# Performance work log

Hardware: AMD Instinct MI355X
Metric: run time of the kernel (lower is better)

Reference implementation:

```python
import jax, jax.numpy as jnp
import numpy as np

DIM = 1024
NUM_HEADS = 16
REL_DIM = 32
B, N = 8, 512


def setup_inputs() -> dict:
    key = jax.random.key(0)
    ks = jax.random.split(key, 8)
    s = 0.02
    return {
        "x": jax.random.normal(ks[0], (B, N, DIM), dtype=jnp.float32),
        "rel_bias": jax.random.normal(ks[1], (B, N, N, REL_DIM), dtype=jnp.float32),
        # torch nn.Linear convention: weight (out_features, in_features)
        "W_qkv": jax.random.normal(ks[2], (3 * DIM, DIM), dtype=jnp.float32) * s,
        "b_qkv": jax.random.normal(ks[3], (3 * DIM,), dtype=jnp.float32) * s,
        "W_rel": jax.random.normal(ks[4], (NUM_HEADS, REL_DIM), dtype=jnp.float32) * s,
        "b_rel": jax.random.normal(ks[5], (NUM_HEADS,), dtype=jnp.float32) * s,
        "W_out": jax.random.normal(ks[6], (DIM, DIM), dtype=jnp.float32) * s,
        "b_out": jax.random.normal(ks[7], (DIM,), dtype=jnp.float32) * s,
    }


def reference(x, rel_bias, W_qkv, b_qkv, W_rel, b_rel, W_out, b_out):
    Bx, Nx, D = x.shape
    H = NUM_HEADS
    hd = D // H
    # QKV projection: (B,N,3D) -> (B,N,3,H,hd)
    qkv = (x @ W_qkv.T + b_qkv).reshape(Bx, Nx, 3, H, hd)
    q, k, v = qkv[:, :, 0], qkv[:, :, 1], qkv[:, :, 2]
    scale = hd ** -0.5
    attn = jnp.einsum('bnhd,bmhd->bhnm', q, k) * scale
    # per-pair relative bias projected to heads: (B,N,N,H) -> (B,H,N,N)
    rel = (rel_bias @ W_rel.T + b_rel).transpose(0, 3, 1, 2)
    attn = jax.nn.softmax(attn + rel, axis=-1)
    out = jnp.einsum('bhnm,bmhd->bnhd', attn, v).reshape(Bx, Nx, D)
    return out @ W_out.T + b_out
```

## Files before the change

kernel.cpp:

```cpp
#include <hip/hip_runtime.h>

typedef unsigned short u16;
typedef unsigned int u32;
typedef __attribute__((ext_vector_type(8))) __bf16 bf16x8;
typedef __attribute__((ext_vector_type(4))) float f32x4;

union U8 {
  bf16x8 b;
  uint2 u2[2];
  uint4 u4;
  u16 us[8];
};

__device__ __forceinline__ u16 f2bf(float f) {
  u32 x = __float_as_uint(f);
  x += 0x7FFFu + ((x >> 16) & 1u);
  return (u16)(x >> 16);
}
__device__ __forceinline__ float bf2f(u16 u) {
  return __uint_as_float(((u32)u) << 16);
}

#define GLOAD16(gp, lp)                                                          \
  __builtin_amdgcn_global_load_lds(                                              \
      (const __attribute__((address_space(1))) unsigned int*)(const void*)(gp),  \
      (__attribute__((address_space(3))) unsigned int*)(void*)(lp), 16, 0, 0)

__global__ void k_convert_all(const float* __restrict__ x, const float* __restrict__ wq,
                              const float* __restrict__ wo, u16* __restrict__ xb,
                              u16* __restrict__ wqb, u16* __restrict__ wob) {
  const int NX = 1048576, NQ = 786432, NO = 262144;
  int idx = blockIdx.x * blockDim.x + threadIdx.x;
  int stride = gridDim.x * blockDim.x;
  for (int i = idx; i < NX + NQ + NO; i += stride) {
    const float4* s;
    ushort4* d;
    int k;
    if (i < NX) { s = (const float4*)x; d = (ushort4*)xb; k = i; }
    else if (i < NX + NQ) { s = (const float4*)wq; d = (ushort4*)wqb; k = i - NX; }
    else { s = (const float4*)wo; d = (ushort4*)wob; k = i - NX - NQ; }
    float4 v = s[k];
    ushort4 o;
    o.x = f2bf(v.x); o.y = f2bf(v.y); o.z = f2bf(v.z); o.w = f2bf(v.w);
    d[k] = o;
  }
}

__global__ __launch_bounds__(256) void k_rel(const float* __restrict__ rb,
                                             const float* __restrict__ Wr,
                                             const float* __restrict__ br,
                                             u16* __restrict__ out) {
  __shared__ float Wl[16][32];
  __shared__ float bl[16];
  int t = threadIdx.x;
  ((float*)Wl)[t] = Wr[t];
  ((float*)Wl)[t + 256] = Wr[t + 256];
  if (t < 16) bl[t] = br[t];
  __syncthreads();

  const int i16 = t & 15, j = (t >> 4) & 3, c = t >> 6;
  const int mt = blockIdx.x, ntg = blockIdx.y, b = blockIdx.z;
  const int nt = ntg >> 2, g = ntg & 3;
  const int n = nt * 16 + 4 * g + j;
  const int m = mt * 64 + c * 16 + i16;

  const float4* rp = (const float4*)(rb + ((size_t)(b * 512 + n) * 512 + m) * 32);
  float4 r4[8];
#pragma unroll
  for (int q = 0; q < 8; ++q) r4[q] = rp[q];

  const size_t obase =
      (((size_t)(b * 16) * 32 + nt) * 8 + mt) * 1024 + c * 256 + (g * 16 + i16) * 4 + j;
#pragma unroll
  for (int h = 0; h < 16; ++h) {
    float acc = bl[h];
    const float* w = Wl[h];
#pragma unroll
    for (int q = 0; q < 8; ++q) {
      acc += r4[q].x * w[4 * q + 0] + r4[q].y * w[4 * q + 1] +
             r4[q].z * w[4 * q + 2] + r4[q].w * w[4 * q + 3];
    }
    out[obase + (size_t)h * 262144] = f2bf(acc);
  }
}

template <int MODE>
__global__ __launch_bounds__(256) void k_gemm(const u16* __restrict__ A,
                                              const u16* __restrict__ Bm,
                                              const float* __restrict__ bias,
                                              u16* __restrict__ Qo, u16* __restrict__ Ko,
                                              u16* __restrict__ Vo, float* __restrict__ Co,
                                              int K) {
  __shared__ u16 Al[128 * 64];
  __shared__ u16 Bl[128 * 64];
  const int t = threadIdx.x;
  const int lane = t & 63, wid = t >> 6;
  const int g = lane >> 4, i16 = lane & 15;
  const int wm = wid >> 1, wn = wid & 1;
  const int bm = blockIdx.y, bn = blockIdx.x;

  f32x4 zero = {0.f, 0.f, 0.f, 0.f};
  f32x4 acc[4][4];
#pragma unroll
  for (int mi = 0; mi < 4; ++mi)
#pragma unroll
    for (int ni = 0; ni < 4; ++ni) acc[mi][ni] = zero;

  int srow[4], sgc[4];
#pragma unroll
  for (int i = 0; i < 4; ++i) {
    int ch = wid * 256 + i * 64 + lane;
    int r = ch >> 3, cs = ch & 7;
    srow[i] = r;
    sgc[i] = cs ^ (r & 7);
  }

  for (int k0 = 0; k0 < K; k0 += 64) {
    __syncthreads();
#pragma unroll
    for (int i = 0; i < 4; ++i) {
      const u16* ga = A + (size_t)(bm * 128 + srow[i]) * K + k0 + sgc[i] * 8;
      const u16* gb = Bm + (size_t)(bn * 128 + srow[i]) * K + k0 + sgc[i] * 8;
      GLOAD16(ga, Al + (size_t)(wid * 256 + i * 64) * 8);
      GLOAD16(gb, Bl + (size_t)(wid * 256 + i * 64) * 8);
    }
    __syncthreads();

#pragma unroll
    for (int kk = 0; kk < 2; ++kk) {
      U8 af[4], bfr[4];
#pragma unroll
      for (int mi = 0; mi < 4; ++mi) {
        int row = wm * 64 + mi * 16 + i16;
        int ch = (g + 4 * kk) ^ (row & 7);
        af[mi].u4 = *(const uint4*)(Al + row * 64 + ch * 8);
      }
#pragma unroll
      for (int ni = 0; ni < 4; ++ni) {
        int row = wn * 64 + ni * 16 + i16;
        int ch = (g + 4 * kk) ^ (row & 7);
        bfr[ni].u4 = *(const uint4*)(Bl + row * 64 + ch * 8);
      }
#pragma unroll
      for (int mi = 0; mi < 4; ++mi)
#pragma unroll
        for (int ni = 0; ni < 4; ++ni)
          acc[mi][ni] = __builtin_amdgcn_mfma_f32_16x16x32_bf16(af[mi].b, bfr[ni].b,
                                                                acc[mi][ni], 0, 0, 0);
    }
  }

#pragma unroll
  for (int mi = 0; mi < 4; ++mi) {
#pragma unroll
    for (int ni = 0; ni < 4; ++ni) {
      int colb = bn * 128 + wn * 64 + ni * 16;
      int col = colb + i16;
#pragma unroll
      for (int j = 0; j < 4; ++j) {
        int row = bm * 128 + wm * 64 + mi * 16 + 4 * g + j;
        float v = acc[mi][ni][j] + bias[col];
        if (MODE == 0) {
          int tt = col >> 10;
          int h = (col >> 6) & 15;
          int d = col & 63;
          int b = row >> 9;
          int n = row & 511;
          u16* dst = (tt == 0) ? Qo : ((tt == 1) ? Ko : Vo);
          dst[((size_t)(b * 16 + h) * 512 + n) * 64 + d] = f2bf(v);
        } else {
          Co[(size_t)row * 1024 + col] = v;
        }
      }
    }
  }
}

__global__ __launch_bounds__(256) void k_vt(const u16* __restrict__ V, u16* __restrict__ Vt) {
  __shared__ u16 Tl[64][72];
  const int t = threadIdx.x;
  const int n0 = blockIdx.x * 64;
  const size_t bh = blockIdx.y;
#pragma unroll
  for (int i = 0; i < 2; ++i) {
    int c = i * 256 + t;
    int r = c >> 3, c8 = (c & 7) * 8;
    U8 v;
    v.u4 = *(const uint4*)(V + (bh * 512 + n0 + r) * 64 + c8);
    *(uint2*)&Tl[r][c8] = v.u2[0];
    *(uint2*)&Tl[r][c8 + 4] = v.u2[1];
  }
  __syncthreads();
#pragma unroll
  for (int i = 0; i < 2; ++i) {
    int c = i * 256 + t;
    int d = c >> 3, n8 = (c & 7) * 8;
    U8 o;
#pragma unroll
    for (int j = 0; j < 8; ++j) o.us[j] = Tl[n8 + j][d];
    *(uint4*)(Vt + (bh * 64 + d) * 512 + n0 + n8) = o.u4;
  }
}

__global__ __launch_bounds__(256) void k_attn(const u16* __restrict__ Q,
                                              const u16* __restrict__ Kb,
                                              const u16* __restrict__ Vtb,
                                              const u16* __restrict__ Rel,
                                              u16* __restrict__ Out) {
  __shared__ u16 Kl[2][64 * 64];
  __shared__ u16 Vl[2][64 * 64];
  __shared__ u16 Pl[4][16 * 68];

  const int qt = blockIdx.x, h = blockIdx.y, b = blockIdx.z;
  const int t = threadIdx.x, lane = t & 63, wid = t >> 6;
  const int g = lane >> 4, i16 = lane & 15;
  const size_t bh = (size_t)(b * 16 + h);

  const u16* Qg = Q + (bh * 512 + qt * 64 + wid * 16 + i16) * 64;
  U8 qf[2];
  qf[0].u4 = *(const uint4*)(Qg + 8 * g);
  qf[1].u4 = *(const uint4*)(Qg + 8 * g + 32);

  float m_run[4], l_run[4];
  f32x4 zero = {0.f, 0.f, 0.f, 0.f};
  f32x4 acc[4];
#pragma unroll
  for (int c = 0; c < 4; ++c) acc[c] = zero;
#pragma unroll
  for (int j = 0; j < 4; ++j) { m_run[j] = -1e30f; l_run[j] = 0.f; }

  int srow[2], sgc[2];
#pragma unroll
  for (int i = 0; i < 2; ++i) {
    int ch = wid * 128 + i * 64 + lane;
    int r = ch >> 3, cs = ch & 7;
    srow[i] = r;
    sgc[i] = cs ^ (r & 7);
  }

  const u16* Kg0 = Kb + bh * 512 * 64;
  const u16* Vg0 = Vtb + bh * 64 * 512;
  const u16* Rg = Rel + ((bh * 32 + qt * 4 + wid) * 8) * 1024 + lane * 4;

#define STAGE(buf, m0)                                                                  \
  do {                                                                                  \
    _Pragma("unroll") for (int i = 0; i < 2; ++i) {                                     \
      GLOAD16(Kg0 + (size_t)((m0) + srow[i]) * 64 + sgc[i] * 8,                         \
              &Kl[buf][(size_t)(wid * 128 + i * 64) * 8]);                              \
      GLOAD16(Vg0 + (size_t)srow[i] * 512 + (m0) + sgc[i] * 8,                          \
              &Vl[buf][(size_t)(wid * 128 + i * 64) * 8]);                              \
    }                                                                                   \
  } while (0)

  STAGE(0, 0);
  __syncthreads();

  for (int it = 0; it < 8; ++it) {
    const int buf = it & 1;
    if (it < 7) STAGE(buf ^ 1, it * 64 + 64);

    uint2 rl[4];
#pragma unroll
    for (int c = 0; c < 4; ++c) rl[c] = *(const uint2*)(Rg + it * 1024 + c * 256);

    f32x4 s[4];
#pragma unroll
    for (int c = 0; c < 4; ++c) s[c] = zero;
    __builtin_amdgcn_s_setprio(1);
#pragma unroll
    for (int c = 0; c < 4; ++c) {
#pragma unroll
      for (int kk = 0; kk < 2; ++kk) {
        int row = c * 16 + i16;
        int ch = (g + 4 * kk) ^ (row & 7);
        U8 kf;
        kf.u4 = *(const uint4*)(&Kl[buf][row * 64 + ch * 8]);
        s[c] = __builtin_amdgcn_mfma_f32_16x16x32_bf16(qf[kk].b, kf.b, s[c], 0, 0, 0);
      }
    }
    __builtin_amdgcn_s_setprio(0);

#pragma unroll
    for (int c = 0; c < 4; ++c) {
      const u16* rc = (const u16*)&rl[c];
#pragma unroll
      for (int j = 0; j < 4; ++j) s[c][j] = s[c][j] * 0.125f + bf2f(rc[j]);
    }
    float fac[4];
#pragma unroll
    for (int j = 0; j < 4; ++j) {
      float pm = fmaxf(fmaxf(s[0][j], s[1][j]), fmaxf(s[2][j], s[3][j]));
      pm = fmaxf(pm, __shfl_xor(pm, 1));
      pm = fmaxf(pm, __shfl_xor(pm, 2));
      pm = fmaxf(pm, __shfl_xor(pm, 4));
      pm = fmaxf(pm, __shfl_xor(pm, 8));
      float mnew = fmaxf(m_run[j], pm);
      fac[j] = __expf(m_run[j] - mnew);
      m_run[j] = mnew;
    }
#pragma unroll
    for (int c = 0; c < 4; ++c)
#pragma unroll
      for (int j = 0; j < 4; ++j) s[c][j] = __expf(s[c][j] - m_run[j]);
#pragma unroll
    for (int j = 0; j < 4; ++j) {
      float rs = s[0][j] + s[1][j] + s[2][j] + s[3][j];
      rs += __shfl_xor(rs, 1);
      rs += __shfl_xor(rs, 2);
      rs += __shfl_xor(rs, 4);
      rs += __shfl_xor(rs, 8);
      l_run[j] = l_run[j] * fac[j] + rs;
    }
#pragma unroll
    for (int c = 0; c < 4; ++c)
#pragma unroll
      for (int j = 0; j < 4; ++j) acc[c][j] *= fac[j];

    u16* Pw = Pl[wid];
#pragma unroll
    for (int c = 0; c < 4; ++c)
#pragma unroll
      for (int j = 0; j < 4; ++j)
        Pw[(4 * g + j) * 68 + c * 16 + i16] = f2bf(s[c][j]);
    __syncthreads();

    U8 pf[2];
#pragma unroll
    for (int kk = 0; kk < 2; ++kk) {
      const u16* p = Pl[wid] + i16 * 68 + 8 * g + 32 * kk;
      pf[kk].u2[0] = *(const uint2*)p;
      pf[kk].u2[1] = *(const uint2*)(p + 4);
    }
    __builtin_amdgcn_s_setprio(1);
#pragma unroll
    for (int c = 0; c < 4; ++c) {
#pragma unroll
      for (int kk = 0; kk < 2; ++kk) {
        int row = c * 16 + i16;
        int ch = (g + 4 * kk) ^ (row & 7);
        U8 vf;
        vf.u4 = *(const uint4*)(&Vl[buf][row * 64 + ch * 8]);
        acc[c] = __builtin_amdgcn_mfma_f32_16x16x32_bf16(pf[kk].b, vf.b, acc[c], 0, 0, 0);
      }
    }
    __builtin_amdgcn_s_setprio(0);
    __syncthreads();
  }
#undef STAGE

#pragma unroll
  for (int c = 0; c < 4; ++c) {
#pragma unroll
    for (int j = 0; j < 4; ++j) {
      int n = qt * 64 + wid * 16 + 4 * g + j;
      float v = acc[c][j] / l_run[j];
      Out[((size_t)b * 512 + n) * 1024 + h * 64 + c * 16 + i16] = f2bf(v);
    }
  }
}

extern "C" void kernel_launch(void* const* d_in, const int* in_sizes, int n_in,
                              void* d_out, int out_size, void* d_ws, size_t ws_size,
                              hipStream_t stream) {
  const float* x = (const float*)d_in[0];
  const float* rel_bias = (const float*)d_in[1];
  const float* W_qkv = (const float*)d_in[2];
  const float* b_qkv = (const float*)d_in[3];
  const float* W_rel = (const float*)d_in[4];
  const float* b_rel = (const float*)d_in[5];
  const float* W_out = (const float*)d_in[6];
  const float* b_out = (const float*)d_in[7];
  float* out = (float*)d_out;

  char* ws = (char*)d_ws;
  u16* x_bf    = (u16*)(ws);
  u16* Vt      = (u16*)(ws);
  u16* wqkv_bf = (u16*)(ws + 8388608);
  u16* wout_bf = (u16*)(ws + 14680064);
  u16* Qw      = (u16*)(ws + 16777216);
  u16* Kw      = (u16*)(ws + 25165824);
  u16* Vw      = (u16*)(ws + 33554432);
  u16* relb    = (u16*)(ws + 41943040);
  u16* attno   = (u16*)(ws + 109051904);

  k_convert_all<<<2048, 256, 0, stream>>>(x, W_qkv, W_out, x_bf, wqkv_bf, wout_bf);

  k_rel<<<dim3(8, 128, 8), 256, 0, stream>>>(rel_bias, W_rel, b_rel, relb);

  k_gemm<0><<<dim3(24, 32), 256, 0, stream>>>(x_bf, wqkv_bf, b_qkv, Qw, Kw, Vw, nullptr, 1024);

  k_vt<<<dim3(8, 128), 256, 0, stream>>>(Vw, Vt);

  k_attn<<<dim3(8, 16, 8), 256, 0, stream>>>(Qw, Kw, Vt, relb, attno);

  k_gemm<1><<<dim3(8, 32), 256, 0, stream>>>(attno, wout_bf, b_out, nullptr, nullptr, nullptr,
                                             out, 1024);
}
```

Measured before the change: 202.4 us.

## Fuse V transpose into QKV GEMM epilogue and read rel weights directly

The QKV GEMM epilogue now writes V directly in transposed (d-major) layout, packing four consecutive rows into one 8-byte store, so the separate k_vt transpose kernel and its launch and round trip through memory are removed. k_rel drops its shared-memory staging of W_rel/b_rel and the block barrier, reading the weights directly from global memory, where they are expected to hit in cache. Writing V transposed gives strided, less coalesced stores in the GEMM epilogue, and the direct weight reads may add scalar or vector loads in place of LDS reads.

```diff
diff --git a/kernel.cpp b/kernel.cpp
--- a/kernel.cpp
+++ b/kernel.cpp
@@ -50,14 +50,7 @@
                                              const float* __restrict__ Wr,
                                              const float* __restrict__ br,
                                              u16* __restrict__ out) {
-  __shared__ float Wl[16][32];
-  __shared__ float bl[16];
-  int t = threadIdx.x;
-  ((float*)Wl)[t] = Wr[t];
-  ((float*)Wl)[t + 256] = Wr[t + 256];
-  if (t < 16) bl[t] = br[t];
-  __syncthreads();
-
+  const int t = threadIdx.x;
   const int i16 = t & 15, j = (t >> 4) & 3, c = t >> 6;
   const int mt = blockIdx.x, ntg = blockIdx.y, b = blockIdx.z;
   const int nt = ntg >> 2, g = ntg & 3;
@@ -73,8 +66,8 @@
       (((size_t)(b * 16) * 32 + nt) * 8 + mt) * 1024 + c * 256 + (g * 16 + i16) * 4 + j;
 #pragma unroll
   for (int h = 0; h < 16; ++h) {
-    float acc = bl[h];
-    const float* w = Wl[h];
+    float acc = br[h];
+    const float* w = Wr + h * 32;
 #pragma unroll
     for (int q = 0; q < 8; ++q) {
       acc += r4[q].x * w[4 * q + 0] + r4[q].y * w[4 * q + 1] +
@@ -154,51 +147,32 @@
   for (int mi = 0; mi < 4; ++mi) {
 #pragma unroll
     for (int ni = 0; ni < 4; ++ni) {
-      int colb = bn * 128 + wn * 64 + ni * 16;
-      int col = colb + i16;
-#pragma unroll
-      for (int j = 0; j < 4; ++j) {
-        int row = bm * 128 + wm * 64 + mi * 16 + 4 * g + j;
-        float v = acc[mi][ni][j] + bias[col];
-        if (MODE == 0) {
-          int tt = col >> 10;
-          int h = (col >> 6) & 15;
-          int d = col & 63;
-          int b = row >> 9;
-          int n = row & 511;
-          u16* dst = (tt == 0) ? Qo : ((tt == 1) ? Ko : Vo);
-          dst[((size_t)(b * 16 + h) * 512 + n) * 64 + d] = f2bf(v);
+      int col = bn * 128 + wn * 64 + ni * 16 + i16;
+      int row0 = bm * 128 + wm * 64 + mi * 16 + 4 * g;
+      float bia = bias[col];
+      if (MODE == 0) {
+        int tt = col >> 10;
+        int h = (col >> 6) & 15;
+        int d = col & 63;
+        int b = row0 >> 9;
+        int n0 = row0 & 511;
+        if (tt < 2) {
+          u16* dst = (tt == 0) ? Qo : Ko;
+#pragma unroll
+          for (int j = 0; j < 4; ++j)
+            dst[((size_t)(b * 16 + h) * 512 + n0 + j) * 64 + d] = f2bf(acc[mi][ni][j] + bia);
         } else {
-          Co[(size_t)row * 1024 + col] = v;
+          uint2 w;
+          w.x = (u32)f2bf(acc[mi][ni][0] + bia) | ((u32)f2bf(acc[mi][ni][1] + bia) << 16);
+          w.y = (u32)f2bf(acc[mi][ni][2] + bia) | ((u32)f2bf(acc[mi][ni][3] + bia) << 16);
+          *(uint2*)(Vo + ((size_t)(b * 16 + h) * 64 + d) * 512 + n0) = w;
         }
-      }
-    }
-  }
-}
-
-__global__ __launch_bounds__(256) void k_vt(const u16* __restrict__ V, u16* __restrict__ Vt) {
-  __shared__ u16 Tl[64][72];
-  const int t = threadIdx.x;
-  const int n0 = blockIdx.x * 64;
-  const size_t bh = blockIdx.y;
-#pragma unroll
-  for (int i = 0; i < 2; ++i) {
-    int c = i * 256 + t;
-    int r = c >> 3, c8 = (c & 7) * 8;
-    U8 v;
-    v.u4 = *(const uint4*)(V + (bh * 512 + n0 + r) * 64 + c8);
-    *(uint2*)&Tl[r][c8] = v.u2[0];
-    *(uint2*)&Tl[r][c8 + 4] = v.u2[1];
-  }
-  __syncthreads();
-#pragma unroll
-  for (int i = 0; i < 2; ++i) {
-    int c = i * 256 + t;
-    int d = c >> 3, n8 = (c & 7) * 8;
-    U8 o;
-#pragma unroll
-    for (int j = 0; j < 8; ++j) o.us[j] = Tl[n8 + j][d];
-    *(uint4*)(Vt + (bh * 64 + d) * 512 + n0 + n8) = o.u4;
+      } else {
+#pragma unroll
+        for (int j = 0; j < 4; ++j)
+          Co[(size_t)(row0 + j) * 1024 + col] = acc[mi][ni][j] + bia;
+      }
+    }
   }
 }
 
@@ -374,12 +348,11 @@
 
   char* ws = (char*)d_ws;
   u16* x_bf    = (u16*)(ws);
-  u16* Vt      = (u16*)(ws);
   u16* wqkv_bf = (u16*)(ws + 8388608);
   u16* wout_bf = (u16*)(ws + 14680064);
   u16* Qw      = (u16*)(ws + 16777216);
   u16* Kw      = (u16*)(ws + 25165824);
-  u16* Vw      = (u16*)(ws + 33554432);
+  u16* Vt      = (u16*)(ws + 33554432);
   u16* relb    = (u16*)(ws + 41943040);
   u16* attno   = (u16*)(ws + 109051904);
 
@@ -387,9 +360,7 @@
 
   k_rel<<<dim3(8, 128, 8), 256, 0, stream>>>(rel_bias, W_rel, b_rel, relb);
 
-  k_gemm<0><<<dim3(24, 32), 256, 0, stream>>>(x_bf, wqkv_bf, b_qkv, Qw, Kw, Vw, nullptr, 1024);
-
-  k_vt<<<dim3(8, 128), 256, 0, stream>>>(Vw, Vt);
+  k_gemm<0><<<dim3(24, 32), 256, 0, stream>>>(x_bf, wqkv_bf, b_qkv, Qw, Kw, Vt, nullptr, 1024);
 
   k_attn<<<dim3(8, 16, 8), 256, 0, stream>>>(Qw, Kw, Vt, relb, attno);
 
```

Result: faster. 186.8 us (-7.7%).
